# Optimization experiments

Hardware: AMD Instinct MI355X
Metric: run time of the kernel (lower is better)

## Reference

```python
import jax, jax.numpy as jnp
import numpy as np

NUM_COMPONENTS = 4
HEADS = 16

def setup_inputs() -> dict:
    key = jax.random.key(0)
    ks = jax.random.split(key, 7)
    BC, S, D = 8, 4096, 1024   # batch*components, latent tokens, hidden dim
    E = 160                     # encoder (text) sequence length
    w_scale = 0.02              # keep logits in a sane range
    return {
        "hidden_states": jax.random.normal(ks[0], (BC, S, D), jnp.float32),
        "encoder_hidden_states": jax.random.normal(ks[1], (BC, E, D), jnp.float32),
        "Wq": jax.random.normal(ks[2], (D, D), jnp.float32) * w_scale,
        "Wk": jax.random.normal(ks[3], (D, D), jnp.float32) * w_scale,
        "Wv": jax.random.normal(ks[4], (D, D), jnp.float32) * w_scale,
        "Wo": jax.random.normal(ks[5], (D, D), jnp.float32) * w_scale,
        "bo": jnp.zeros((D,), jnp.float32),
    }

def reference(hidden_states, encoder_hidden_states, Wq, Wk, Wv, Wo, bo):
    BC, S, D = hidden_states.shape
    E = encoder_hidden_states.shape[1]
    C = NUM_COMPONENTS
    B = BC // C
    H = HEADS
    dh = D // H
    scale = dh ** -0.5

    # projections (diffusers to_q/to_k/to_v, no bias)
    q = hidden_states @ Wq            # [BC, S, D]
    k = encoder_hidden_states @ Wk    # [BC, E, D]
    v = encoder_hidden_states @ Wv    # [BC, E, D]

    q = q.reshape(BC, S, H, dh).transpose(0, 2, 1, 3)  # [BC, H, S, dh]
    k = k.reshape(BC, E, H, dh).transpose(0, 2, 1, 3)  # [BC, H, E, dh]
    v = v.reshape(BC, E, H, dh).transpose(0, 2, 1, 3)  # [BC, H, E, dh]

    scores = jnp.einsum("bhsd,bhtd->bhst", q, k) * scale  # [BC, H, S, E]
    scores_c = scores.reshape(C, B, H, S, E)

    # pooled (mean over encoder tokens) softmax across components
    pooled = scores_c.mean(axis=-1, keepdims=True)         # [C, B, H, S, 1]
    weights_pooled = jax.nn.softmax(pooled, axis=0)        # softmax over components
    # per-row softmax over encoder tokens, scaled by component weight
    weights = jax.nn.softmax(scores_c, axis=-1) * weights_pooled
    weights = weights.reshape(BC, H, S, E)

    out = jnp.einsum("bhst,bhtd->bhsd", weights, v)        # [BC, H, S, dh]
    out = out.transpose(0, 2, 1, 3).reshape(BC, S, D)

    out = out @ Wo + bo        # to_out[0]; to_out[1] is dropout (identity, eval)
    out = out + hidden_states  # residual_connection=True, rescale factor 1
    return out
```

## Files before the change

kernel.cpp:

```cpp
#include <hip/hip_runtime.h>
#include <stdint.h>

typedef __attribute__((ext_vector_type(8))) short short8;
typedef __attribute__((ext_vector_type(4))) float f32x4;
typedef __attribute__((ext_vector_type(4))) unsigned short us4;

#define DI __device__ __forceinline__

static constexpr int Dm = 1024;
static constexpr int Sm = 4096;
static constexpr int Em = 160;
static constexpr int Hm = 16;

static constexpr size_t OFF_HSB  = 0;
static constexpr size_t OFF_WT   = 67108864;
static constexpr size_t OFF_QB   = 75497472;
static constexpr size_t OFF_KB   = 142606336;
static constexpr size_t OFF_VT   = 147849216;
static constexpr size_t OFF_EHSB = 150994944;

DI unsigned short f2b(float f) {
  union { float f; unsigned u; } x; x.f = f;
  unsigned r = x.u + 0x7fffu + ((x.u >> 16) & 1u);
  return (unsigned short)(r >> 16);
}

DI void gl_lds16(const void* g, void* l) {
  __builtin_amdgcn_global_load_lds(
      (const __attribute__((address_space(1))) unsigned int*)g,
      (__attribute__((address_space(3))) unsigned int*)l, 16, 0, 0);
}

__global__ void k_cvt(const float* __restrict__ in, unsigned short* __restrict__ out, int n4) {
  int stride = gridDim.x * blockDim.x;
  for (int i = blockIdx.x * blockDim.x + threadIdx.x; i < n4; i += stride) {
    float4 v = ((const float4*)in)[i];
    us4 o = { f2b(v.x), f2b(v.y), f2b(v.z), f2b(v.w) };
    *(us4*)(out + (size_t)i * 4) = o;
  }
}

__global__ void k_wtrans(const float* __restrict__ W0, const float* __restrict__ W1,
                         const float* __restrict__ W2, const float* __restrict__ W3,
                         unsigned short* __restrict__ Wt) {
  __shared__ float t[32][33];
  const float* W = (blockIdx.z == 0) ? W0 : (blockIdx.z == 1) ? W1 : (blockIdx.z == 2) ? W2 : W3;
  unsigned short* o = Wt + (size_t)blockIdx.z * 1048576;
  int tx = threadIdx.x, ty = threadIdx.y;
  int n = blockIdx.x * 32 + tx;
  int k0 = blockIdx.y * 32;
  #pragma unroll
  for (int j = ty; j < 32; j += 8) t[j][tx] = W[(size_t)(k0 + j) * 1024 + n];
  __syncthreads();
  #pragma unroll
  for (int j = ty; j < 32; j += 8)
    o[(size_t)(blockIdx.x * 32 + j) * 1024 + k0 + tx] = f2b(t[tx][j]);
}

template<int MODE>
__global__ __launch_bounds__(512, 2) void k_gemm256(const unsigned short* __restrict__ A,
                                                    const unsigned short* __restrict__ Bt,
                                                    void* __restrict__ Cout,
                                                    const float* __restrict__ bias,
                                                    const float* __restrict__ resid) {
  __shared__ __align__(16) char smem[131072];
  const int tid = threadIdx.x;
  const int lane = tid & 63;
  const int l15 = lane & 15;
  const int g = lane >> 4;
  const int wv = tid >> 6;
  const int wr = wv >> 2;
  const int wcn = wv & 3;
  const int bid = blockIdx.x;
  const int m0 = (((bid >> 5) << 3) + (bid & 7)) * 256;
  const int n0 = ((bid >> 3) & 3) * 256;

  f32x4 acc[8][4];
  #pragma unroll
  for (int i = 0; i < 8; ++i)
    #pragma unroll
    for (int j = 0; j < 4; ++j) acc[i][j] = (f32x4){0.f, 0.f, 0.f, 0.f};

  auto STAGE = [&](int bb, int t) {
    #pragma unroll
    for (int ps = 0; ps < 4; ++ps) {
      int ch = ps * 512 + tid;
      int row = ch >> 3, j = ch & 7;
      int sj = (j ^ (row & 7)) * 8;
      gl_lds16(A  + (size_t)(m0 + row) * 1024 + t * 64 + sj, smem + bb * 32768 + ch * 16);
      gl_lds16(Bt + (size_t)(n0 + row) * 1024 + t * 64 + sj, smem + 65536 + bb * 32768 + ch * 16);
    }
  };

  STAGE(0, 0);
  int cb = 0;
  for (int t = 0; t < 16; ++t) {
    __syncthreads();
    if (t < 15) STAGE(cb ^ 1, t + 1);
    const char* Ab = smem + cb * 32768;
    const char* Bb = smem + 65536 + cb * 32768;
    #pragma unroll
    for (int ph = 0; ph < 4; ++ph) {
      const int mh = ph >> 1;
      const int nh = (ph >> 1) ^ (ph & 1);
      short8 af[2][4], bf[2][2];
      #pragma unroll
      for (int kk = 0; kk < 2; ++kk) {
        #pragma unroll
        for (int mt = 0; mt < 4; ++mt)
          af[kk][mt] = *(const short8*)(Ab + (wr * 128 + mh * 64 + mt * 16 + l15) * 128 +
                                        ((kk * 64 + g * 16) ^ ((l15 & 7) << 4)));
        #pragma unroll
        for (int nt = 0; nt < 2; ++nt)
          bf[kk][nt] = *(const short8*)(Bb + (wcn * 64 + nh * 32 + nt * 16 + l15) * 128 +
                                        ((kk * 64 + g * 16) ^ ((l15 & 7) << 4)));
      }
      __builtin_amdgcn_sched_barrier(0);
      __builtin_amdgcn_s_setprio(1);
      #pragma unroll
      for (int kk = 0; kk < 2; ++kk)
        #pragma unroll
        for (int mt = 0; mt < 4; ++mt)
          #pragma unroll
          for (int nt = 0; nt < 2; ++nt)
            acc[mh * 4 + mt][nh * 2 + nt] = __builtin_amdgcn_mfma_f32_16x16x32_bf16(
                af[kk][mt], bf[kk][nt], acc[mh * 4 + mt][nh * 2 + nt], 0, 0, 0);
      __builtin_amdgcn_s_setprio(0);
      __builtin_amdgcn_sched_barrier(0);
    }
    cb ^= 1;
  }

  #pragma unroll
  for (int m = 0; m < 8; ++m)
    #pragma unroll
    for (int n = 0; n < 4; ++n)
      #pragma unroll
      for (int r = 0; r < 4; ++r) {
        size_t row = (size_t)(m0 + wr * 128 + m * 16 + 4 * g + r);
        int col = n0 + wcn * 64 + n * 16 + l15;
        size_t idx = row * 1024 + col;
        if (MODE == 0) ((unsigned short*)Cout)[idx] = f2b(acc[m][n][r]);
        else           ((float*)Cout)[idx] = acc[m][n][r] + bias[col] + resid[idx];
      }
}

__global__ __launch_bounds__(256, 2) void k_gemm_kv(const unsigned short* __restrict__ A,
                                                    const unsigned short* __restrict__ Wt,
                                                    unsigned short* __restrict__ kb,
                                                    unsigned short* __restrict__ vt) {
  __shared__ __align__(16) char smem[32768];
  char* As = smem;
  char* Bs = smem + 16384;
  const int tid = threadIdx.x;
  const int lane = tid & 63;
  const int l15 = lane & 15;
  const int g = lane >> 4;
  const int wv = tid >> 6;
  const int wr = wv >> 1, wc = wv & 1;
  const int m0 = blockIdx.x * 128, n0 = blockIdx.y * 128;
  const int z = blockIdx.z;
  const unsigned short* Bt = Wt + (size_t)(1 + z) * 1048576;

  f32x4 acc[4][4];
  #pragma unroll
  for (int i = 0; i < 4; ++i)
    #pragma unroll
    for (int j = 0; j < 4; ++j) acc[i][j] = (f32x4){0.f, 0.f, 0.f, 0.f};

  for (int t = 0; t < 16; ++t) {
    __syncthreads();
    #pragma unroll
    for (int is = 0; is < 4; ++is) {
      int ch = is * 256 + tid;
      int row = ch >> 3, j = ch & 7;
      int sj = (j ^ (row & 7)) * 8;
      gl_lds16(A  + (size_t)(m0 + row) * 1024 + t * 64 + sj, As + ch * 16);
      gl_lds16(Bt + (size_t)(n0 + row) * 1024 + t * 64 + sj, Bs + ch * 16);
    }
    __syncthreads();
    short8 af[2][4], bf[2][4];
    #pragma unroll
    for (int kk = 0; kk < 2; ++kk)
      #pragma unroll
      for (int mt = 0; mt < 4; ++mt) {
        af[kk][mt] = *(const short8*)(As + (wr * 64 + mt * 16 + l15) * 128 + ((kk * 64 + g * 16) ^ ((l15 & 7) << 4)));
        bf[kk][mt] = *(const short8*)(Bs + (wc * 64 + mt * 16 + l15) * 128 + ((kk * 64 + g * 16) ^ ((l15 & 7) << 4)));
      }
    #pragma unroll
    for (int kk = 0; kk < 2; ++kk)
      #pragma unroll
      for (int mt = 0; mt < 4; ++mt)
        #pragma unroll
        for (int nt = 0; nt < 4; ++nt)
          acc[mt][nt] = __builtin_amdgcn_mfma_f32_16x16x32_bf16(af[kk][mt], bf[kk][nt], acc[mt][nt], 0, 0, 0);
  }

  #pragma unroll
  for (int mt = 0; mt < 4; ++mt)
    #pragma unroll
    for (int nt = 0; nt < 4; ++nt)
      #pragma unroll
      for (int r = 0; r < 4; ++r) {
        int row = m0 + wr * 64 + mt * 16 + 4 * g + r;
        int col = n0 + wc * 64 + nt * 16 + l15;
        unsigned short hv = f2b(acc[mt][nt][r]);
        if (z == 0) {
          kb[(size_t)row * 1024 + col] = hv;
        } else {
          int bc = row / 160, e = row - bc * 160;
          vt[((size_t)(bc * 16 + (col >> 6)) * 64 + (col & 63)) * 192 + e] = hv;
        }
      }
}

__global__ __launch_bounds__(256, 2) void k_attn(const unsigned short* __restrict__ Qb,
                                                 const unsigned short* __restrict__ Kb,
                                                 const unsigned short* __restrict__ Vt,
                                                 unsigned short* __restrict__ AOb) {
  __shared__ __align__(16) char smem[22528];
  float* pooled = (float*)(smem + 21504);
  const int tid = threadIdx.x, lane = tid & 63, wv = tid >> 6;
  const int g = lane >> 4, l15 = lane & 15;
  const int s0 = blockIdx.x * 64;
  const int h = blockIdx.y;
  const int b = blockIdx.z;
  const int bc = wv * 2 + b;
  const float scale = 0.125f;

  const unsigned short* Qp = Qb + ((size_t)bc * Sm + s0) * Dm + h * 64;
  const unsigned short* Kp = Kb + (size_t)bc * Em * Dm + h * 64;
  const unsigned short* Vp = Vt + ((size_t)bc * Hm + h) * (64 * 192);
  unsigned short* Op = AOb + ((size_t)bc * Sm + s0) * Dm + h * 64;
  char* Pw = smem + wv * 5376;

  #pragma unroll 1
  for (int st = 0; st < 4; ++st) {
    short8 qf[2];
    #pragma unroll
    for (int kk = 0; kk < 2; ++kk)
      qf[kk] = *(const short8*)(Qp + (size_t)(st * 16 + l15) * Dm + kk * 32 + g * 8);
    f32x4 sc[10];
    #pragma unroll
    for (int et = 0; et < 10; ++et) {
      sc[et] = (f32x4){0.f, 0.f, 0.f, 0.f};
      #pragma unroll
      for (int kk = 0; kk < 2; ++kk) {
        short8 kf = *(const short8*)(Kp + (size_t)(et * 16 + l15) * Dm + kk * 32 + g * 8);
        sc[et] = __builtin_amdgcn_mfma_f32_16x16x32_bf16(qf[kk], kf, sc[et], 0, 0, 0);
      }
    }
    float rs4[4];
    #pragma unroll
    for (int r = 0; r < 4; ++r) {
      float v = 0.f;
      #pragma unroll
      for (int et = 0; et < 10; ++et) v += sc[et][r];
      v += __shfl_xor(v, 1); v += __shfl_xor(v, 2); v += __shfl_xor(v, 4); v += __shfl_xor(v, 8);
      if (l15 == 0) pooled[(st * 16 + 4 * g + r) * 4 + wv] = v * (scale / 160.f);
      float mx = sc[0][r];
      #pragma unroll
      for (int et = 1; et < 10; ++et) mx = fmaxf(mx, sc[et][r]);
      mx = fmaxf(mx, __shfl_xor(mx, 1)); mx = fmaxf(mx, __shfl_xor(mx, 2));
      mx = fmaxf(mx, __shfl_xor(mx, 4)); mx = fmaxf(mx, __shfl_xor(mx, 8));
      float rs = 0.f;
      #pragma unroll
      for (int et = 0; et < 10; ++et) {
        float p = __expf((sc[et][r] - mx) * scale);
        rs += p;
        *(unsigned short*)(Pw + (4 * g + r) * 336 + (et * 16 + l15) * 2) = f2b(p);
      }
      rs += __shfl_xor(rs, 1); rs += __shfl_xor(rs, 2); rs += __shfl_xor(rs, 4); rs += __shfl_xor(rs, 8);
      rs4[r] = rs;
    }
    f32x4 oa[4];
    #pragma unroll
    for (int dt = 0; dt < 4; ++dt) oa[dt] = (f32x4){0.f, 0.f, 0.f, 0.f};
    #pragma unroll
    for (int k5 = 0; k5 < 5; ++k5) {
      short8 pf = *(const short8*)(Pw + l15 * 336 + k5 * 64 + g * 16);
      #pragma unroll
      for (int dt = 0; dt < 4; ++dt) {
        short8 vf = *(const short8*)(Vp + (size_t)(dt * 16 + l15) * 192 + k5 * 32 + g * 8);
        oa[dt] = __builtin_amdgcn_mfma_f32_16x16x32_bf16(pf, vf, oa[dt], 0, 0, 0);
      }
    }
    __syncthreads();
    #pragma unroll
    for (int r = 0; r < 4; ++r) {
      float4 pl = *(const float4*)&pooled[(st * 16 + 4 * g + r) * 4];
      float m3 = fmaxf(fmaxf(pl.x, pl.y), fmaxf(pl.z, pl.w));
      float ssum = __expf(pl.x - m3) + __expf(pl.y - m3) + __expf(pl.z - m3) + __expf(pl.w - m3);
      float mine = (wv == 0) ? pl.x : (wv == 1) ? pl.y : (wv == 2) ? pl.z : pl.w;
      float srw = __expf(mine - m3) / (ssum * rs4[r]);
      #pragma unroll
      for (int dt = 0; dt < 4; ++dt)
        Op[(size_t)(st * 16 + 4 * g + r) * Dm + dt * 16 + l15] = f2b(oa[dt][r] * srw);
    }
  }
}

extern "C" void kernel_launch(void* const* d_in, const int* in_sizes, int n_in,
                              void* d_out, int out_size, void* d_ws, size_t ws_size,
                              hipStream_t stream) {
  const float* hs  = (const float*)d_in[0];
  const float* ehs = (const float*)d_in[1];
  const float* Wq  = (const float*)d_in[2];
  const float* Wk  = (const float*)d_in[3];
  const float* Wv  = (const float*)d_in[4];
  const float* Wo  = (const float*)d_in[5];
  const float* bo  = (const float*)d_in[6];
  char* ws = (char*)d_ws;
  unsigned short* hsb = (unsigned short*)(ws + OFF_HSB);
  unsigned short* wt  = (unsigned short*)(ws + OFF_WT);
  unsigned short* qb  = (unsigned short*)(ws + OFF_QB);
  unsigned short* kb  = (unsigned short*)(ws + OFF_KB);
  unsigned short* vt  = (unsigned short*)(ws + OFF_VT);
  unsigned short* eb  = (unsigned short*)(ws + OFF_EHSB);

  hipLaunchKernelGGL(k_cvt, dim3(1280), dim3(256), 0, stream, ehs, eb, 8 * 160 * 1024 / 4);
  hipLaunchKernelGGL(k_wtrans, dim3(32, 32, 4), dim3(32, 8), 0, stream, Wq, Wk, Wv, Wo, wt);
  hipLaunchKernelGGL(k_gemm_kv, dim3(10, 8, 2), dim3(256), 0, stream, eb, wt, kb, vt);
  hipLaunchKernelGGL(k_cvt, dim3(2048), dim3(256), 0, stream, hs, hsb, 8 * 4096 * 1024 / 4);
  hipLaunchKernelGGL((k_gemm256<0>), dim3(512), dim3(512), 0, stream, hsb, wt, (void*)qb,
                     (const float*)nullptr, (const float*)nullptr);
  hipLaunchKernelGGL(k_attn, dim3(64, 16, 2), dim3(256), 0, stream, qb, kb, vt, hsb);
  hipLaunchKernelGGL((k_gemm256<1>), dim3(512), dim3(512), 0, stream, hsb, wt + 3 * 1048576, d_out, bo, hs);
}
```

Baseline: 351.9 us.

## Interleave half-tile staging with MFMA phases in big GEMM; stage bf16 epilogue through LDS

```diff
diff --git a/kernel.cpp b/kernel.cpp
--- a/kernel.cpp
+++ b/kernel.cpp
@@ -30,6 +30,9 @@
       (const __attribute__((address_space(1))) unsigned int*)g,
       (__attribute__((address_space(3))) unsigned int*)l, 16, 0, 0);
 }
+
+#define S_BARRIER __builtin_amdgcn_s_barrier()
+#define LGKM0 do { asm volatile("s_waitcnt lgkmcnt(0)" ::: "memory"); __builtin_amdgcn_sched_barrier(0); } while (0)
 
 __global__ void k_cvt(const float* __restrict__ in, unsigned short* __restrict__ out, int n4) {
   int stride = gridDim.x * blockDim.x;
@@ -81,68 +84,135 @@
     #pragma unroll
     for (int j = 0; j < 4; ++j) acc[i][j] = (f32x4){0.f, 0.f, 0.f, 0.f};
 
-  auto STAGE = [&](int bb, int t) {
-    #pragma unroll
-    for (int ps = 0; ps < 4; ++ps) {
-      int ch = ps * 512 + tid;
-      int row = ch >> 3, j = ch & 7;
-      int sj = (j ^ (row & 7)) * 8;
-      gl_lds16(A  + (size_t)(m0 + row) * 1024 + t * 64 + sj, smem + bb * 32768 + ch * 16);
-      gl_lds16(Bt + (size_t)(n0 + row) * 1024 + t * 64 + sj, smem + 65536 + bb * 32768 + ch * 16);
+  auto STG = [&](const unsigned short* G, int isB, int db, int hf, int tk) {
+    int mn0 = isB ? n0 : m0;
+    #pragma unroll
+    for (int p = 0; p < 2; ++p) {
+      int chl = p * 512 + tid;
+      int rih = chl >> 3, j = chl & 7;
+      int sj = (j ^ (rih & 7)) * 8;
+      gl_lds16(G + (size_t)(mn0 + hf * 128 + rih) * 1024 + tk * 64 + sj,
+               smem + isB * 65536 + db * 32768 + (hf * 1024 + chl) * 16);
     }
   };
-
-  STAGE(0, 0);
-  int cb = 0;
-  for (int t = 0; t < 16; ++t) {
-    __syncthreads();
-    if (t < 15) STAGE(cb ^ 1, t + 1);
-    const char* Ab = smem + cb * 32768;
-    const char* Bb = smem + 65536 + cb * 32768;
-    #pragma unroll
-    for (int ph = 0; ph < 4; ++ph) {
-      const int mh = ph >> 1;
-      const int nh = (ph >> 1) ^ (ph & 1);
-      short8 af[2][4], bf[2][2];
-      #pragma unroll
-      for (int kk = 0; kk < 2; ++kk) {
-        #pragma unroll
-        for (int mt = 0; mt < 4; ++mt)
-          af[kk][mt] = *(const short8*)(Ab + (wr * 128 + mh * 64 + mt * 16 + l15) * 128 +
-                                        ((kk * 64 + g * 16) ^ ((l15 & 7) << 4)));
+  auto LDA = [&](short8 (&af)[2][4], int db, int mh) {
+    const char* buf = smem + db * 32768;
+    #pragma unroll
+    for (int kk = 0; kk < 2; ++kk)
+      #pragma unroll
+      for (int mt = 0; mt < 4; ++mt)
+        af[kk][mt] = *(const short8*)(buf + (wr * 128 + mh * 64 + mt * 16 + l15) * 128 +
+                                      ((kk * 64 + g * 16) ^ ((l15 & 7) << 4)));
+  };
+  auto LDB = [&](short8 (&bf)[2][2], int db, int nh) {
+    const char* buf = smem + 65536 + db * 32768;
+    #pragma unroll
+    for (int kk = 0; kk < 2; ++kk)
+      #pragma unroll
+      for (int nt = 0; nt < 2; ++nt)
+        bf[kk][nt] = *(const short8*)(buf + (wcn * 64 + nh * 32 + nt * 16 + l15) * 128 +
+                                      ((kk * 64 + g * 16) ^ ((l15 & 7) << 4)));
+  };
+  auto MM = [&](short8 (&af)[2][4], short8 (&bf)[2][2], int mh, int nh) {
+    __builtin_amdgcn_s_setprio(1);
+    #pragma unroll
+    for (int kk = 0; kk < 2; ++kk)
+      #pragma unroll
+      for (int mt = 0; mt < 4; ++mt)
         #pragma unroll
         for (int nt = 0; nt < 2; ++nt)
-          bf[kk][nt] = *(const short8*)(Bb + (wcn * 64 + nh * 32 + nt * 16 + l15) * 128 +
-                                        ((kk * 64 + g * 16) ^ ((l15 & 7) << 4)));
-      }
-      __builtin_amdgcn_sched_barrier(0);
-      __builtin_amdgcn_s_setprio(1);
-      #pragma unroll
-      for (int kk = 0; kk < 2; ++kk)
+          acc[mh * 4 + mt][nh * 2 + nt] = __builtin_amdgcn_mfma_f32_16x16x32_bf16(
+              af[kk][mt], bf[kk][nt], acc[mh * 4 + mt][nh * 2 + nt], 0, 0, 0);
+    __builtin_amdgcn_s_setprio(0);
+    __builtin_amdgcn_sched_barrier(0);
+  };
+
+  STG(A, 0, 0, 0, 0); STG(Bt, 1, 0, 0, 0); STG(Bt, 1, 0, 1, 0); STG(A, 0, 0, 1, 0);
+  STG(A, 0, 1, 0, 1); STG(Bt, 1, 1, 1, 1); STG(A, 0, 1, 1, 1);
+  asm volatile("s_waitcnt vmcnt(6)" ::: "memory");
+  S_BARRIER;
+
+  short8 af[2][4], bf0[2][2], bf1[2][2];
+  #pragma unroll 1
+  for (int v = 0; v < 8; ++v) {
+    const int t = 2 * v;
+    const bool more = (v < 7);
+    LDA(af, 0, 0); LDB(bf0, 0, 0);
+    STG(Bt, 1, 1, 0, t + 1);
+    S_BARRIER; LGKM0;
+    MM(af, bf0, 0, 0);
+    S_BARRIER;
+    LDB(bf1, 0, 1);
+    if (more) STG(A, 0, 0, 0, t + 2);
+    S_BARRIER; LGKM0;
+    MM(af, bf1, 0, 1);
+    S_BARRIER;
+    LDA(af, 0, 1);
+    if (more) STG(Bt, 1, 0, 1, t + 2);
+    S_BARRIER; LGKM0;
+    MM(af, bf1, 1, 1);
+    S_BARRIER;
+    LDB(bf0, 0, 0);
+    if (more) STG(A, 0, 0, 1, t + 2);
+    S_BARRIER; LGKM0;
+    MM(af, bf0, 1, 0);
+    if (more) { asm volatile("s_waitcnt vmcnt(6)" ::: "memory"); }
+    else      { asm volatile("s_waitcnt vmcnt(0)" ::: "memory"); }
+    S_BARRIER;
+    LDA(af, 1, 0); LDB(bf0, 1, 0);
+    if (more) STG(Bt, 1, 0, 0, t + 2);
+    S_BARRIER; LGKM0;
+    MM(af, bf0, 0, 0);
+    S_BARRIER;
+    LDB(bf1, 1, 1);
+    if (more) STG(A, 0, 1, 0, t + 3);
+    S_BARRIER; LGKM0;
+    MM(af, bf1, 0, 1);
+    S_BARRIER;
+    LDA(af, 1, 1);
+    if (more) STG(Bt, 1, 1, 1, t + 3);
+    S_BARRIER; LGKM0;
+    MM(af, bf1, 1, 1);
+    S_BARRIER;
+    LDB(bf0, 1, 0);
+    if (more) STG(A, 0, 1, 1, t + 3);
+    S_BARRIER; LGKM0;
+    MM(af, bf0, 1, 0);
+    asm volatile("s_waitcnt vmcnt(6)" ::: "memory");
+    S_BARRIER;
+  }
+
+  __syncthreads();
+  if (MODE == 0) {
+    unsigned short* Cl = (unsigned short*)smem;
+    #pragma unroll
+    for (int m = 0; m < 8; ++m)
+      #pragma unroll
+      for (int n = 0; n < 4; ++n)
         #pragma unroll
-        for (int mt = 0; mt < 4; ++mt)
-          #pragma unroll
-          for (int nt = 0; nt < 2; ++nt)
-            acc[mh * 4 + mt][nh * 2 + nt] = __builtin_amdgcn_mfma_f32_16x16x32_bf16(
-                af[kk][mt], bf[kk][nt], acc[mh * 4 + mt][nh * 2 + nt], 0, 0, 0);
-      __builtin_amdgcn_s_setprio(0);
-      __builtin_amdgcn_sched_barrier(0);
-    }
-    cb ^= 1;
-  }
-
-  #pragma unroll
-  for (int m = 0; m < 8; ++m)
-    #pragma unroll
-    for (int n = 0; n < 4; ++n)
-      #pragma unroll
-      for (int r = 0; r < 4; ++r) {
-        size_t row = (size_t)(m0 + wr * 128 + m * 16 + 4 * g + r);
-        int col = n0 + wcn * 64 + n * 16 + l15;
-        size_t idx = row * 1024 + col;
-        if (MODE == 0) ((unsigned short*)Cout)[idx] = f2b(acc[m][n][r]);
-        else           ((float*)Cout)[idx] = acc[m][n][r] + bias[col] + resid[idx];
-      }
+        for (int r = 0; r < 4; ++r)
+          Cl[(wr * 128 + m * 16 + 4 * g + r) * 256 + wcn * 64 + n * 16 + l15] = f2b(acc[m][n][r]);
+    __syncthreads();
+    #pragma unroll
+    for (int j = 0; j < 16; ++j) {
+      int ch = j * 512 + tid;
+      int row = ch >> 5, sl = ch & 31;
+      *(short8*)((unsigned short*)Cout + (size_t)(m0 + row) * 1024 + n0 + sl * 8) =
+          *(const short8*)(Cl + row * 256 + sl * 8);
+    }
+  } else {
+    #pragma unroll
+    for (int m = 0; m < 8; ++m)
+      #pragma unroll
+      for (int n = 0; n < 4; ++n)
+        #pragma unroll
+        for (int r = 0; r < 4; ++r) {
+          size_t row = (size_t)(m0 + wr * 128 + m * 16 + 4 * g + r);
+          int col = n0 + wcn * 64 + n * 16 + l15;
+          size_t idx = row * 1024 + col;
+          ((float*)Cout)[idx] = acc[m][n][r] + bias[col] + resid[idx];
+        }
+  }
 }
 
 __global__ __launch_bounds__(256, 2) void k_gemm_kv(const unsigned short* __restrict__ A,
```

New measurement: 349.8 us. No clear change (-0.6%).
